# Kernel optimization log

Measured on AMD Instinct MI355X. Metric: run time of the kernel, lower is better.

Reference implementation:

```python
import jax, jax.numpy as jnp
import numpy as np
from jax import lax

WINDOW_SIZE = 12
POOL = 4  # AvgPool2d(4): 12x12 -> 3x3

# 4 directional 3x3 kernels, stacked as [O=4, I=1, 3, 3]
_KERNELS = np.stack([
    np.array([[0, 0, 0], [-1, 1, 0], [0, 0, 0]], np.float32),  # left
    np.array([[0, 0, 0], [0, 1, -1], [0, 0, 0]], np.float32),  # right
    np.array([[0, -1, 0], [0, 1, 0], [0, 0, 0]], np.float32),  # up
    np.array([[0, 0, 0], [0, 1, 0], [0, -1, 0]], np.float32),  # down
])[:, None, :, :]


def setup_inputs() -> dict:
    key = jax.random.key(0)
    k1, k2 = jax.random.split(key)
    windows_num = 200000
    n = WINDOW_SIZE * WINDOW_SIZE * windows_num
    samples1 = jax.random.uniform(k1, (n, 3), dtype=jnp.float32)
    samples2 = jax.random.uniform(k2, (n, 3), dtype=jnp.float32)
    return {"samples1": samples1, "samples2": samples2, "windows_num": windows_num}


def _to_pooled(samples, windows_num):
    # [W*W*N, C] -> [W, W, N, C] -> [N, C, W, W]
    x = samples.reshape(WINDOW_SIZE, WINDOW_SIZE, windows_num, -1)
    x = jnp.transpose(x, (2, 3, 0, 1))
    # channel mean, keepdim -> [N, 1, W, W]
    m = jnp.mean(x, axis=1, keepdims=True)
    # AvgPool2d(4): [N,1,12,12] -> [N,1,3,3]
    hp = WINDOW_SIZE // POOL
    p = m.reshape(windows_num, 1, hp, POOL, hp, POOL).mean(axis=(3, 5))
    return p


def _dir_grads(x):
    # x: [N,1,3,3]; 4 directional 3x3 convs, padding=1 -> [N,4,3,3]
    k = jnp.asarray(_KERNELS)
    return lax.conv_general_dilated(
        x, k, window_strides=(1, 1), padding=[(1, 1), (1, 1)],
        dimension_numbers=("NCHW", "OIHW", "NCHW"))


def reference(samples1, samples2, windows_num):
    org_pool = _to_pooled(samples1, windows_num)
    enh_pool = _to_pooled(samples2, windows_num)
    d_org = _dir_grads(org_pool)
    d_enh = _dir_grads(enh_pool)
    # squared diff per direction, summed over the 4 directions -> [N,3,3]
    E = jnp.sum((d_org - d_enh) ** 2, axis=1)
    return jnp.mean(E)
```

## Files before the change

kernel.cpp:

```cpp
#include <hip/hip_runtime.h>

typedef float f32x4 __attribute__((ext_vector_type(4)));

__global__ __launch_bounds__(64) void spa_kernel_v4(
    const float* __restrict__ s1, const float* __restrict__ s2,
    float* __restrict__ out, int N, float scale) {
  const int g4 = blockIdx.x * 64 + (int)threadIdx.x;
  const int nG = N >> 2;

  float P[4][9];
#pragma unroll
  for (int w = 0; w < 4; ++w)
#pragma unroll
    for (int k = 0; k < 9; ++k) P[w][k] = 0.f;

  if (g4 < nG) {
    const size_t stride = (size_t)N * 3u;
    const float* p1 = s1 + (size_t)g4 * 12u;
    const float* p2 = s2 + (size_t)g4 * 12u;
#pragma unroll 1
    for (int i = 0; i < 12; ++i) {
      const int pr = (i >> 2) * 3;
#pragma unroll
      for (int j = 0; j < 12; ++j) {
        const f32x4* a = (const f32x4*)(p1 + (size_t)j * stride);
        const f32x4* b = (const f32x4*)(p2 + (size_t)j * stride);
        f32x4 a0 = __builtin_nontemporal_load(a);
        f32x4 a1 = __builtin_nontemporal_load(a + 1);
        f32x4 a2 = __builtin_nontemporal_load(a + 2);
        f32x4 b0 = __builtin_nontemporal_load(b);
        f32x4 b1 = __builtin_nontemporal_load(b + 1);
        f32x4 b2 = __builtin_nontemporal_load(b + 2);
        float d0 = (a0.x + a0.y + a0.z) - (b0.x + b0.y + b0.z);
        float d1 = (a0.w + a1.x + a1.y) - (b0.w + b1.x + b1.y);
        float d2 = (a1.z + a1.w + a2.x) - (b1.z + b1.w + b2.x);
        float d3 = (a2.y + a2.z + a2.w) - (b2.y + b2.z + b2.w);
        const int pc = pr + (j >> 2);
        P[0][pc] += d0;
        P[1][pc] += d1;
        P[2][pc] += d2;
        P[3][pc] += d3;
      }
      p1 += (size_t)12 * stride;
      p2 += (size_t)12 * stride;
    }
  }

  float e = 0.f;
#pragma unroll
  for (int w = 0; w < 4; ++w) {
    float Q[9];
#pragma unroll
    for (int k = 0; k < 9; ++k) Q[k] = P[w][k] * (1.0f / 48.0f);
#pragma unroll
    for (int i = 0; i < 3; ++i)
#pragma unroll
      for (int j = 0; j < 3; ++j) {
        float c = Q[i * 3 + j];
        float l = (j > 0) ? Q[i * 3 + j - 1] : 0.f;
        float r = (j < 2) ? Q[i * 3 + j + 1] : 0.f;
        float u = (i > 0) ? Q[(i - 1) * 3 + j] : 0.f;
        float d = (i < 2) ? Q[(i + 1) * 3 + j] : 0.f;
        float dl = c - l, dr = c - r, du = c - u, dd = c - d;
        e += dl * dl + dr * dr + du * du + dd * dd;
      }
  }

#pragma unroll
  for (int off = 32; off > 0; off >>= 1) e += __shfl_down(e, off, 64);
  if ((threadIdx.x & 63) == 0) atomicAdd(out, e * scale);
}

__global__ __launch_bounds__(512) void spa_kernel_s(
    const float* __restrict__ s1, const float* __restrict__ s2,
    float* __restrict__ out, int N, float scale) {
  const int win = blockIdx.x * 512 + threadIdx.x;
  float P[9];
#pragma unroll
  for (int k = 0; k < 9; ++k) P[k] = 0.f;

  if (win < N) {
    const size_t stride = (size_t)N * 3u;
    const float* p1 = s1 + (size_t)win * 3u;
    const float* p2 = s2 + (size_t)win * 3u;
#pragma unroll 1
    for (int i = 0; i < 12; ++i) {
      const int pr = (i >> 2) * 3;
#pragma unroll
      for (int j = 0; j < 12; ++j) {
        const float* a = p1 + (size_t)j * stride;
        const float* b = p2 + (size_t)j * stride;
        float d = (a[0] + a[1] + a[2]) - (b[0] + b[1] + b[2]);
        P[pr + (j >> 2)] += d;
      }
      p1 += (size_t)12 * stride;
      p2 += (size_t)12 * stride;
    }
  }

#pragma unroll
  for (int k = 0; k < 9; ++k) P[k] *= (1.0f / 48.0f);

  float e = 0.f;
#pragma unroll
  for (int i = 0; i < 3; ++i)
#pragma unroll
    for (int j = 0; j < 3; ++j) {
      float c = P[i * 3 + j];
      float l = (j > 0) ? P[i * 3 + j - 1] : 0.f;
      float r = (j < 2) ? P[i * 3 + j + 1] : 0.f;
      float u = (i > 0) ? P[(i - 1) * 3 + j] : 0.f;
      float d = (i < 2) ? P[(i + 1) * 3 + j] : 0.f;
      float dl = c - l, dr = c - r, du = c - u, dd = c - d;
      e += dl * dl + dr * dr + du * du + dd * dd;
    }

  const int lane = threadIdx.x & 63;
  const int wid = threadIdx.x >> 6;
#pragma unroll
  for (int off = 32; off > 0; off >>= 1) e += __shfl_down(e, off, 64);

  __shared__ float sPart[8];
  if (lane == 0) sPart[wid] = e;
  __syncthreads();
  if (threadIdx.x == 0) {
    float t = 0.f;
#pragma unroll
    for (int w = 0; w < 8; ++w) t += sPart[w];
    atomicAdd(out, t * scale);
  }
}

extern "C" void kernel_launch(void* const* d_in, const int* in_sizes, int n_in,
                              void* d_out, int out_size, void* d_ws, size_t ws_size,
                              hipStream_t stream) {
  const float* s1 = (const float*)d_in[0];
  const float* s2 = (const float*)d_in[1];
  float* out = (float*)d_out;
  int N = in_sizes[0] / (12 * 12 * 3);
  float scale = 1.0f / (9.0f * (float)N);
  hipMemsetAsync(d_out, 0, sizeof(float), stream);
  if ((N & 3) == 0) {
    int nG = N >> 2;
    int blocks = (nG + 63) / 64;
    spa_kernel_v4<<<blocks, 64, 0, stream>>>(s1, s2, out, N, scale);
  } else {
    int blocks = (N + 511) / 512;
    spa_kernel_s<<<blocks, 512, 0, stream>>>(s1, s2, out, N, scale);
  }
}
```

Measured before the change: 753.0 us.

## Split pooled rows across three wavefronts per block and combine via shared memory

Each block now runs three wavefronts, each handling one pooled row (4 input rows) for the same 64 window groups, instead of one wavefront walking all 12 rows. Partial pooled sums from wavefronts 1 and 2 go through LDS to wavefront 0, which computes the gradient energy and does the atomic add. This triples thread-level parallelism and shortens each thread's serial load chain, aiming for better memory latency hiding on a bandwidth-bound kernel, at the cost of a block-level sync and a small LDS exchange.

After: 737.4 us. 2.1% less time.

```diff
diff --git a/kernel.cpp b/kernel.cpp
--- a/kernel.cpp
+++ b/kernel.cpp
@@ -2,25 +2,27 @@
 
 typedef float f32x4 __attribute__((ext_vector_type(4)));
 
-__global__ __launch_bounds__(64) void spa_kernel_v4(
+__global__ __launch_bounds__(192) void spa_kernel_p3(
     const float* __restrict__ s1, const float* __restrict__ s2,
     float* __restrict__ out, int N, float scale) {
-  const int g4 = blockIdx.x * 64 + (int)threadIdx.x;
-  const int nG = N >> 2;
+  const int lane = threadIdx.x & 63;
+  const int rg   = threadIdx.x >> 6;
+  const int g4   = blockIdx.x * 64 + lane;
+  const int nG   = N >> 2;
 
-  float P[4][9];
+  float P[4][3];
 #pragma unroll
   for (int w = 0; w < 4; ++w)
 #pragma unroll
-    for (int k = 0; k < 9; ++k) P[w][k] = 0.f;
+    for (int c = 0; c < 3; ++c) P[w][c] = 0.f;
 
   if (g4 < nG) {
     const size_t stride = (size_t)N * 3u;
-    const float* p1 = s1 + (size_t)g4 * 12u;
-    const float* p2 = s2 + (size_t)g4 * 12u;
+    const size_t rowoff = (size_t)12 * stride;
+    const float* p1 = s1 + (size_t)g4 * 12u + (size_t)(rg * 4) * rowoff;
+    const float* p2 = s2 + (size_t)g4 * 12u + (size_t)(rg * 4) * rowoff;
 #pragma unroll 1
-    for (int i = 0; i < 12; ++i) {
-      const int pr = (i >> 2) * 3;
+    for (int ii = 0; ii < 4; ++ii) {
 #pragma unroll
       for (int j = 0; j < 12; ++j) {
         const f32x4* a = (const f32x4*)(p1 + (size_t)j * stride);
@@ -35,40 +37,54 @@
         float d1 = (a0.w + a1.x + a1.y) - (b0.w + b1.x + b1.y);
         float d2 = (a1.z + a1.w + a2.x) - (b1.z + b1.w + b2.x);
         float d3 = (a2.y + a2.z + a2.w) - (b2.y + b2.z + b2.w);
-        const int pc = pr + (j >> 2);
+        const int pc = j >> 2;
         P[0][pc] += d0;
         P[1][pc] += d1;
         P[2][pc] += d2;
         P[3][pc] += d3;
       }
-      p1 += (size_t)12 * stride;
-      p2 += (size_t)12 * stride;
+      p1 += rowoff;
+      p2 += rowoff;
     }
   }
 
-  float e = 0.f;
+  __shared__ float sP[2][64][13];
+  if (rg >= 1) {
 #pragma unroll
-  for (int w = 0; w < 4; ++w) {
-    float Q[9];
+    for (int w = 0; w < 4; ++w)
 #pragma unroll
-    for (int k = 0; k < 9; ++k) Q[k] = P[w][k] * (1.0f / 48.0f);
+      for (int c = 0; c < 3; ++c) sP[rg - 1][lane][w * 3 + c] = P[w][c];
+  }
+  __syncthreads();
+
+  if (rg == 0) {
+    float e = 0.f;
 #pragma unroll
-    for (int i = 0; i < 3; ++i)
+    for (int w = 0; w < 4; ++w) {
+      float Q[9];
 #pragma unroll
-      for (int j = 0; j < 3; ++j) {
-        float c = Q[i * 3 + j];
-        float l = (j > 0) ? Q[i * 3 + j - 1] : 0.f;
-        float r = (j < 2) ? Q[i * 3 + j + 1] : 0.f;
-        float u = (i > 0) ? Q[(i - 1) * 3 + j] : 0.f;
-        float d = (i < 2) ? Q[(i + 1) * 3 + j] : 0.f;
-        float dl = c - l, dr = c - r, du = c - u, dd = c - d;
-        e += dl * dl + dr * dr + du * du + dd * dd;
+      for (int c = 0; c < 3; ++c) {
+        Q[c]     = P[w][c] * (1.0f / 48.0f);
+        Q[3 + c] = sP[0][lane][w * 3 + c] * (1.0f / 48.0f);
+        Q[6 + c] = sP[1][lane][w * 3 + c] * (1.0f / 48.0f);
       }
+#pragma unroll
+      for (int i = 0; i < 3; ++i)
+#pragma unroll
+        for (int j = 0; j < 3; ++j) {
+          float cc = Q[i * 3 + j];
+          float l = (j > 0) ? Q[i * 3 + j - 1] : 0.f;
+          float r = (j < 2) ? Q[i * 3 + j + 1] : 0.f;
+          float u = (i > 0) ? Q[(i - 1) * 3 + j] : 0.f;
+          float d = (i < 2) ? Q[(i + 1) * 3 + j] : 0.f;
+          float dl = cc - l, dr = cc - r, du = cc - u, dd = cc - d;
+          e += dl * dl + dr * dr + du * du + dd * dd;
+        }
+    }
+#pragma unroll
+    for (int off = 32; off > 0; off >>= 1) e += __shfl_down(e, off, 64);
+    if (lane == 0) atomicAdd(out, e * scale);
   }
-
-#pragma unroll
-  for (int off = 32; off > 0; off >>= 1) e += __shfl_down(e, off, 64);
-  if ((threadIdx.x & 63) == 0) atomicAdd(out, e * scale);
 }
 
 __global__ __launch_bounds__(512) void spa_kernel_s(
@@ -143,7 +159,7 @@
   if ((N & 3) == 0) {
     int nG = N >> 2;
     int blocks = (nG + 63) / 64;
-    spa_kernel_v4<<<blocks, 64, 0, stream>>>(s1, s2, out, N, scale);
+    spa_kernel_p3<<<blocks, 192, 0, stream>>>(s1, s2, out, N, scale);
   } else {
     int blocks = (N + 511) / 512;
     spa_kernel_s<<<blocks, 512, 0, stream>>>(s1, s2, out, N, scale);
```
